# Optimization experiments

Measured on AMD Instinct MI355X. Metric: run time of the kernel, lower is better.

Reference implementation:

```python
import jax, jax.numpy as jnp
import numpy as np
import math

B, T, D, H = 2, 2048, 1024, 16
DH = D // H

def setup_inputs() -> dict:
    key = jax.random.key(0)
    ks = jax.random.split(key, 7)
    s = 0.02
    return {
        "q": jax.random.normal(ks[0], (B, T, D), jnp.float32),
        "k": jax.random.normal(ks[1], (B, T, D), jnp.float32),
        "v": jax.random.normal(ks[2], (B, T, D), jnp.float32),
        "wq": jax.random.normal(ks[3], (D, D), jnp.float32) * s,
        "wk": jax.random.normal(ks[4], (D, D), jnp.float32) * s,
        "wv": jax.random.normal(ks[5], (D, D), jnp.float32) * s,
        "wo": jax.random.normal(ks[6], (D, D), jnp.float32) * s,
    }

def reference(q, k, v, wq, wk, wv, wo):
    # nn.Linear(bias=False): y = x @ W.T
    qh = (q @ wq.T).reshape(B, T, H, DH).transpose(0, 2, 1, 3)  # [B,H,T,DH]
    kh = (k @ wk.T).reshape(B, T, H, DH).transpose(0, 2, 1, 3)
    vh = (v @ wv.T).reshape(B, T, H, DH).transpose(0, 2, 1, 3)
    scores = jnp.einsum('bhqd,bhkd->bhqk', qh, kh) / math.sqrt(DH)
    # causal mask: disallow j > i
    mask = jnp.triu(jnp.ones((T, T), dtype=bool), k=1)
    scores = jnp.where(mask[None, None], -jnp.inf, scores)
    attn = jax.nn.softmax(scores, axis=-1)  # dropout=0 (eval)
    out = jnp.einsum('bhqk,bhkd->bhqd', attn, vh)
    out = out.transpose(0, 2, 1, 3).reshape(B, T, D)
    return out @ wo.T
```

## Files before the change

### kernel.cpp

```cpp
#include <hip/hip_runtime.h>
#include <cstdint>
#include <cstddef>

#define B_  2
#define T_  2048
#define D_  1024
#define H_  16
#define DH_ 64
#define M_  (B_*T_)

typedef __bf16 bf16x8 __attribute__((ext_vector_type(8)));
typedef float  f32x4  __attribute__((ext_vector_type(4)));
typedef unsigned short us4 __attribute__((ext_vector_type(4)));
typedef unsigned short us8 __attribute__((ext_vector_type(8)));
typedef unsigned short ushort_t;

__device__ __forceinline__ unsigned short f32_to_bf16_rne(float f) {
    unsigned u = __builtin_bit_cast(unsigned, f);
    u += 0x7FFFu + ((u >> 16) & 1u);
    return (unsigned short)(u >> 16);
}

__device__ __forceinline__ unsigned pack_bf16_2(float f0, float f1) {
    unsigned a = __builtin_bit_cast(unsigned, f0) + 0x8000u;
    unsigned b = __builtin_bit_cast(unsigned, f1) + 0x8000u;
    return __builtin_amdgcn_perm(b, a, 0x07060302u);
}

__device__ __forceinline__ void async16(const void* g, void* l) {
    __builtin_amdgcn_global_load_lds(
        (const __attribute__((address_space(1))) unsigned int*)(uintptr_t)g,
        (__attribute__((address_space(3))) unsigned int*)(uintptr_t)l, 16, 0, 0);
}

__global__ __launch_bounds__(256) void cvt_all(
    const float* __restrict__ i0, const float* __restrict__ i1, const float* __restrict__ i2,
    const float* __restrict__ i3, const float* __restrict__ i4, const float* __restrict__ i5,
    const float* __restrict__ i6,
    ushort_t* __restrict__ o0, ushort_t* __restrict__ o1, ushort_t* __restrict__ o2,
    ushort_t* __restrict__ o3, ushort_t* __restrict__ o4, ushort_t* __restrict__ o5,
    ushort_t* __restrict__ o6) {
    const int y = blockIdx.y;
    const float* in = y == 0 ? i0 : y == 1 ? i1 : y == 2 ? i2 : y == 3 ? i3
                    : y == 4 ? i4 : y == 5 ? i5 : i6;
    ushort_t* out  = y == 0 ? o0 : y == 1 ? o1 : y == 2 ? o2 : y == 3 ? o3
                    : y == 4 ? o4 : y == 5 ? o5 : o6;
    const int n = (y < 3) ? (M_ * D_) : (D_ * D_);
    int i = (blockIdx.x * 256 + threadIdx.x) * 4;
    if (i >= n) return;
    float4 f = *reinterpret_cast<const float4*>(in + i);
    unsigned lo = pack_bf16_2(f.x, f.y);
    unsigned hi = pack_bf16_2(f.z, f.w);
    *reinterpret_cast<unsigned long long*>(out + i) =
        (unsigned long long)lo | ((unsigned long long)hi << 32);
}

__device__ __forceinline__ void gemm_mainloop(const ushort_t* __restrict__ A,
                                              const ushort_t* __restrict__ W,
                                              ushort_t* As, ushort_t* Bs,
                                              int m0, int n0, f32x4 acc[4][4]) {
    const int tid  = threadIdx.x;
    const int lc   = tid & 15;
    const int quad = (tid >> 4) & 3;
    const int wave = tid >> 6;
    const int wm = (wave >> 1) * 64, wn = (wave & 1) * 64;
    const int sw = lc & 7;

    const f32x4 fzero = {0.f, 0.f, 0.f, 0.f};
#pragma unroll
    for (int mt = 0; mt < 4; ++mt)
#pragma unroll
        for (int nt = 0; nt < 4; ++nt) acc[mt][nt] = fzero;

    for (int kk = 0; kk < D_; kk += 64) {
        __syncthreads();
#pragma unroll
        for (int i = 0; i < 4; ++i) {
            const int j = i * 256 + tid;
            const int r = j >> 3, c = (j & 7) ^ (r & 7);
            async16(A + (size_t)(m0 + r) * D_ + kk + c * 8, As + j * 8);
            async16(W + (size_t)(n0 + r) * D_ + kk + c * 8, Bs + j * 8);
        }
        __syncthreads();
#pragma unroll
        for (int ks = 0; ks < 2; ++ks) {
            bf16x8 af[4], bw[4];
#pragma unroll
            for (int mt = 0; mt < 4; ++mt)
                af[mt] = *reinterpret_cast<const bf16x8*>(
                    As + (wm + mt * 16 + lc) * 64 + (((ks * 4 + quad) ^ sw) * 8));
#pragma unroll
            for (int nt = 0; nt < 4; ++nt)
                bw[nt] = *reinterpret_cast<const bf16x8*>(
                    Bs + (wn + nt * 16 + lc) * 64 + (((ks * 4 + quad) ^ sw) * 8));
#pragma unroll
            for (int mt = 0; mt < 4; ++mt)
#pragma unroll
                for (int nt = 0; nt < 4; ++nt)
                    acc[mt][nt] = __builtin_amdgcn_mfma_f32_16x16x32_bf16(af[mt], bw[nt], acc[mt][nt], 0, 0, 0);
        }
    }
}

__global__ __launch_bounds__(256, 3) void gemm_qkv(
    const ushort_t* __restrict__ qb, const ushort_t* __restrict__ kb, const ushort_t* __restrict__ vb,
    const ushort_t* __restrict__ wqb, const ushort_t* __restrict__ wkb, const ushort_t* __restrict__ wvb,
    ushort_t* __restrict__ qhb, ushort_t* __restrict__ khb, ushort_t* __restrict__ vtb) {
    __shared__ __align__(16) ushort_t As[128 * 64];
    __shared__ __align__(16) ushort_t Bs[128 * 64];
    __shared__ __align__(16) ushort_t Ts[4][16 * 80];

    const int z = blockIdx.z;
    const ushort_t* A = z == 0 ? qb : z == 1 ? kb : vb;
    const ushort_t* W = z == 0 ? wqb : z == 1 ? wkb : wvb;
    const int yt = blockIdx.x + 8 * (blockIdx.y >> 3);
    const int xt = blockIdx.y & 7;
    const int m0 = yt * 128, n0 = xt * 128;

    f32x4 acc[4][4];
    gemm_mainloop(A, W, As, Bs, m0, n0, acc);

    const int tid = threadIdx.x, lane = tid & 63, lc = tid & 15;
    const int quad = (tid >> 4) & 3, wave = tid >> 6;
    const int wm = (wave >> 1) * 64, wn = (wave & 1) * 64;
    const int mG = m0 + wm;
    const int bb = mG >> 11, t0 = mG & (T_ - 1);
    const int hh = (n0 + wn) >> 6;

    if (z < 2) {
        ushort_t* outp = (z == 0 ? qhb : khb) + ((size_t)bb * H_ + hh) * T_ * DH_;
#pragma unroll
        for (int mt = 0; mt < 4; ++mt) {
#pragma unroll
            for (int nt = 0; nt < 4; ++nt)
#pragma unroll
                for (int r = 0; r < 4; ++r)
                    Ts[wave][(quad * 4 + r) * 80 + nt * 16 + lc] = f32_to_bf16_rne(acc[mt][nt][r]);
#pragma unroll
            for (int it = 0; it < 2; ++it) {
                const int c = it * 64 + lane;
                const int row = c >> 3, c8 = c & 7;
                us8 vv = *reinterpret_cast<const us8*>(Ts[wave] + row * 80 + c8 * 8);
                *reinterpret_cast<us8*>(outp + (size_t)(t0 + mt * 16 + row) * DH_ + c8 * 8) = vv;
            }
        }
    } else {
        ushort_t* base = vtb + ((size_t)bb * H_ + hh) * DH_ * T_;
#pragma unroll
        for (int mt = 0; mt < 4; ++mt) {
#pragma unroll
            for (int nt = 0; nt < 4; ++nt)
#pragma unroll
                for (int r = 0; r < 4; ++r)
                    Ts[wave][(nt * 16 + lc) * 16 + quad * 4 + r] = f32_to_bf16_rne(acc[mt][nt][r]);
#pragma unroll
            for (int it = 0; it < 2; ++it) {
                const int c = it * 64 + lane;
                const int nl = c >> 1, mh = c & 1;
                us8 vv = *reinterpret_cast<const us8*>(Ts[wave] + c * 8);
                *reinterpret_cast<us8*>(base + (size_t)nl * T_ + t0 + mt * 16 + mh * 8) = vv;
            }
        }
    }
}

__global__ __launch_bounds__(256, 4) void gemm_wo(const ushort_t* __restrict__ A,
                                                  const ushort_t* __restrict__ W,
                                                  float* __restrict__ out) {
    __shared__ __align__(16) ushort_t As[64 * 64];
    __shared__ __align__(16) ushort_t Bs[128 * 64];
    const int yt = blockIdx.x + 8 * (blockIdx.y >> 3);
    const int xt = blockIdx.y & 7;
    const int m0 = yt * 64, n0 = xt * 128;

    const int tid = threadIdx.x, lc = tid & 15;
    const int quad = (tid >> 4) & 3, wave = tid >> 6;
    const int wm = (wave >> 1) * 32, wn = (wave & 1) * 64;
    const int sw = lc & 7;

    const f32x4 fzero = {0.f, 0.f, 0.f, 0.f};
    f32x4 acc[2][4];
#pragma unroll
    for (int mt = 0; mt < 2; ++mt)
#pragma unroll
        for (int nt = 0; nt < 4; ++nt) acc[mt][nt] = fzero;

    for (int kk = 0; kk < D_; kk += 64) {
        __syncthreads();
#pragma unroll
        for (int i = 0; i < 2; ++i) {
            const int j = i * 256 + tid;
            const int r = j >> 3, c = (j & 7) ^ (r & 7);
            async16(A + (size_t)(m0 + r) * D_ + kk + c * 8, As + j * 8);
        }
#pragma unroll
        for (int i = 0; i < 4; ++i) {
            const int j = i * 256 + tid;
            const int r = j >> 3, c = (j & 7) ^ (r & 7);
            async16(W + (size_t)(n0 + r) * D_ + kk + c * 8, Bs + j * 8);
        }
        __syncthreads();
#pragma unroll
        for (int ks = 0; ks < 2; ++ks) {
            bf16x8 af[2], bw[4];
#pragma unroll
            for (int mt = 0; mt < 2; ++mt)
                af[mt] = *reinterpret_cast<const bf16x8*>(
                    As + (wm + mt * 16 + lc) * 64 + (((ks * 4 + quad) ^ sw) * 8));
#pragma unroll
            for (int nt = 0; nt < 4; ++nt)
                bw[nt] = *reinterpret_cast<const bf16x8*>(
                    Bs + (wn + nt * 16 + lc) * 64 + (((ks * 4 + quad) ^ sw) * 8));
#pragma unroll
            for (int mt = 0; mt < 2; ++mt)
#pragma unroll
                for (int nt = 0; nt < 4; ++nt)
                    acc[mt][nt] = __builtin_amdgcn_mfma_f32_16x16x32_bf16(af[mt], bw[nt], acc[mt][nt], 0, 0, 0);
        }
    }

#pragma unroll
    for (int mt = 0; mt < 2; ++mt)
#pragma unroll
        for (int nt = 0; nt < 4; ++nt)
#pragma unroll
            for (int r = 0; r < 4; ++r) {
                const int m = m0 + wm + mt * 16 + quad * 4 + r;
                const int n = n0 + wn + nt * 16 + lc;
                out[(size_t)m * D_ + n] = acc[mt][nt][r];
            }
}

__global__ __launch_bounds__(256, 3) void attn6(const ushort_t* __restrict__ Qh,
                                                const ushort_t* __restrict__ Kh,
                                                const ushort_t* __restrict__ Vt,
                                                ushort_t* __restrict__ Ao) {
    __shared__ __align__(16) ushort_t smem[16384 + 4 * 16 * 72];

    const int tid = threadIdx.x, lane = tid & 63, lc = tid & 15;
    const int quad = (tid >> 4) & 3, wave = tid >> 6;
    const int grp = wave >> 1, sub = wave & 1;
    const int sw = lc & 7;

    const int L = blockIdx.x;
    const int xcd = L & 7, s = L >> 3;
    const int qt = 31 - (s >> 2);
    const int bh = xcd + 8 * (s & 3);
    const int bb = bh >> 4, hh = bh & 15;
    const int q0 = qt * 64, nkt = qt + 1;
    const int nIt = (nkt + 1) >> 1;
    const int mbase = q0 + sub * 32;

    const ushort_t* Qp = Qh + (size_t)bh * T_ * DH_;
    const ushort_t* Kp = Kh + (size_t)bh * T_ * DH_;
    const ushort_t* Vp = Vt + (size_t)bh * DH_ * T_;
    const float SC2 = 0.18033688f;
    const f32x4 fzero = {0.f, 0.f, 0.f, 0.f};
    ushort_t* Pw = smem + 16384 + wave * (16 * 72);

    bf16x8 aq[2][2];
#pragma unroll
    for (int mt = 0; mt < 2; ++mt) {
        const ushort_t* qrow = Qp + (size_t)(mbase + mt * 16 + lc) * DH_ + quad * 8;
        aq[mt][0] = *reinterpret_cast<const bf16x8*>(qrow);
        aq[mt][1] = *reinterpret_cast<const bf16x8*>(qrow + 32);
    }

    f32x4 o[2][4];
    float lsum[2][4];
#pragma unroll
    for (int mt = 0; mt < 2; ++mt) {
#pragma unroll
        for (int ct = 0; ct < 4; ++ct) o[mt][ct] = fzero;
#pragma unroll
        for (int r = 0; r < 4; ++r) lsum[mt][r] = 0.f;
    }

    for (int it = 0; it < nIt; ++it) {
        const int kt0 = 2 * it;
        __syncthreads();
#pragma unroll
        for (int i = 0; i < 2; ++i) {
            const int j = i * 256 + tid;
            const int r = j >> 3, c = (j & 7) ^ (r & 7);
            const int kprm = 4 * (r & 15) + (r >> 4);
            async16(Kp + (size_t)(kt0 * 64 + kprm) * DH_ + c * 8, smem + j * 8);
            async16(Vp + (size_t)r * T_ + kt0 * 64 + c * 8,       smem + 8192 + j * 8);
            if (kt0 + 1 < nkt) {
                async16(Kp + (size_t)((kt0 + 1) * 64 + kprm) * DH_ + c * 8, smem + 4096 + j * 8);
                async16(Vp + (size_t)r * T_ + (kt0 + 1) * 64 + c * 8,       smem + 12288 + j * 8);
            }
        }
        __syncthreads();

        const int kt = kt0 + grp;
        if (kt < nkt) {
            const int k0 = kt * 64;
            const ushort_t* Kt    = smem + grp * 4096;
            const ushort_t* Vtile = smem + 8192 + grp * 4096;

            bf16x8 bv[4][2];
#pragma unroll
            for (int ct = 0; ct < 4; ++ct) {
                const ushort_t* vr = Vtile + (ct * 16 + lc) * 64;
                bv[ct][0] = *reinterpret_cast<const bf16x8*>(vr + ((quad ^ sw) * 8));
                bv[ct][1] = *reinterpret_cast<const bf16x8*>(vr + (((4 + quad) ^ sw) * 8));
            }

            f32x4 sc[2][4];
#pragma unroll
            for (int ct = 0; ct < 4; ++ct) {
                const ushort_t* kr = Kt + (ct * 16 + lc) * 64;
                bf16x8 bk0 = *reinterpret_cast<const bf16x8*>(kr + ((quad ^ sw) * 8));
                bf16x8 bk1 = *reinterpret_cast<const bf16x8*>(kr + (((4 + quad) ^ sw) * 8));
#pragma unroll
                for (int mt = 0; mt < 2; ++mt) {
                    sc[mt][ct] = __builtin_amdgcn_mfma_f32_16x16x32_bf16(aq[mt][0], bk0, fzero, 0, 0, 0);
                    sc[mt][ct] = __builtin_amdgcn_mfma_f32_16x16x32_bf16(aq[mt][1], bk1, sc[mt][ct], 0, 0, 0);
                }
            }

#pragma unroll
            for (int mt = 0; mt < 2; ++mt) {
                float e[4][4];
                if (kt == qt) {
#pragma unroll
                    for (int ct = 0; ct < 4; ++ct) {
                        const int key = k0 + 4 * lc + ct;
#pragma unroll
                        for (int r = 0; r < 4; ++r) {
                            const int row = mbase + mt * 16 + quad * 4 + r;
                            e[ct][r] = (key <= row) ? __builtin_amdgcn_exp2f(sc[mt][ct][r] * SC2) : 0.f;
                        }
                    }
                } else {
#pragma unroll
                    for (int ct = 0; ct < 4; ++ct)
#pragma unroll
                        for (int r = 0; r < 4; ++r)
                            e[ct][r] = __builtin_amdgcn_exp2f(sc[mt][ct][r] * SC2);
                }
#pragma unroll
                for (int r = 0; r < 4; ++r) {
                    lsum[mt][r] += (e[0][r] + e[1][r]) + (e[2][r] + e[3][r]);
                    unsigned lo = pack_bf16_2(e[0][r], e[1][r]);
                    unsigned hi = pack_bf16_2(e[2][r], e[3][r]);
                    *reinterpret_cast<unsigned long long*>(Pw + (quad * 4 + r) * 72 + lc * 4) =
                        (unsigned long long)lo | ((unsigned long long)hi << 32);
                }
                bf16x8 ap0 = *reinterpret_cast<const bf16x8*>(Pw + lc * 72 + quad * 8);
                bf16x8 ap1 = *reinterpret_cast<const bf16x8*>(Pw + lc * 72 + 32 + quad * 8);
#pragma unroll
                for (int ct = 0; ct < 4; ++ct) {
                    o[mt][ct] = __builtin_amdgcn_mfma_f32_16x16x32_bf16(ap0, bv[ct][0], o[mt][ct], 0, 0, 0);
                    o[mt][ct] = __builtin_amdgcn_mfma_f32_16x16x32_bf16(ap1, bv[ct][1], o[mt][ct], 0, 0, 0);
                }
            }
        }
    }

    __syncthreads();
    float* Osh = (float*)smem;
    float* Lsh = (float*)(smem + 8192);
    if (grp == 0) {
#pragma unroll
        for (int mt = 0; mt < 2; ++mt) {
#pragma unroll
            for (int ct = 0; ct < 4; ++ct)
#pragma unroll
                for (int r = 0; r < 4; ++r)
                    Osh[(sub * 32 + mt * 16 + quad * 4 + r) * 64 + ct * 16 + lc] = o[mt][ct][r];
#pragma unroll
            for (int r = 0; r < 4; ++r)
                Lsh[(sub * 32 + mt * 16 + quad * 4 + r) * 16 + lc] = lsum[mt][r];
        }
    }
    __syncthreads();
    if (grp == 1) {
#pragma unroll
        for (int mt = 0; mt < 2; ++mt) {
            float inv[4];
#pragma unroll
            for (int r = 0; r < 4; ++r) {
                float l = lsum[mt][r] + Lsh[(sub * 32 + mt * 16 + quad * 4 + r) * 16 + lc];
#pragma unroll
                for (int d = 1; d < 16; d <<= 1) l += __shfl_xor(l, d);
                inv[r] = 1.0f / l;
            }
#pragma unroll
            for (int ct = 0; ct < 4; ++ct)
#pragma unroll
                for (int r = 0; r < 4; ++r) {
                    const int rowq = mbase + mt * 16 + quad * 4 + r;
                    const float ov = o[mt][ct][r] +
                        Osh[(sub * 32 + mt * 16 + quad * 4 + r) * 64 + ct * 16 + lc];
                    Ao[((size_t)bb * T_ + rowq) * D_ + hh * DH_ + ct * 16 + lc] =
                        f32_to_bf16_rne(ov * inv[r]);
                }
        }
    }
}

extern "C" void kernel_launch(void* const* d_in, const int* in_sizes, int n_in,
                              void* d_out, int out_size, void* d_ws, size_t ws_size,
                              hipStream_t stream) {
    const float* q  = (const float*)d_in[0];
    const float* k  = (const float*)d_in[1];
    const float* v  = (const float*)d_in[2];
    const float* wq = (const float*)d_in[3];
    const float* wk = (const float*)d_in[4];
    const float* wv = (const float*)d_in[5];
    const float* wo = (const float*)d_in[6];

    char* ws = (char*)d_ws;
    size_t off = 0;
    auto alloc = [&](size_t bytes) -> char* {
        char* p = ws + off;
        off += (bytes + 255) & ~(size_t)255;
        return p;
    };
    ushort_t* qb  = (ushort_t*)alloc((size_t)M_ * D_ * 2);
    ushort_t* kb  = (ushort_t*)alloc((size_t)M_ * D_ * 2);
    ushort_t* vb  = (ushort_t*)alloc((size_t)M_ * D_ * 2);
    ushort_t* wqb = (ushort_t*)alloc((size_t)D_ * D_ * 2);
    ushort_t* wkb = (ushort_t*)alloc((size_t)D_ * D_ * 2);
    ushort_t* wvb = (ushort_t*)alloc((size_t)D_ * D_ * 2);
    ushort_t* wob = (ushort_t*)alloc((size_t)D_ * D_ * 2);
    ushort_t* qhb = (ushort_t*)alloc((size_t)M_ * D_ * 2);
    ushort_t* khb = (ushort_t*)alloc((size_t)M_ * D_ * 2);
    ushort_t* vtb = (ushort_t*)alloc((size_t)M_ * D_ * 2);
    ushort_t* aob = (ushort_t*)alloc((size_t)M_ * D_ * 2);

    cvt_all<<<dim3(4096, 7), 256, 0, stream>>>(q, k, v, wq, wk, wv, wo,
                                               qb, kb, vb, wqb, wkb, wvb, wob);

    gemm_qkv<<<dim3(8, 32, 3), 256, 0, stream>>>(qb, kb, vb, wqb, wkb, wvb, qhb, khb, vtb);

    attn6<<<dim3(1024), 256, 0, stream>>>(qhb, khb, vtb, aob);

    gemm_wo<<<dim3(8, 64), 256, 0, stream>>>(aob, wob, (float*)d_out);
}
```

Measured before the change: 187.5 us.

## Register-prefetch next K/V tiles, raise MFMA priority, coalesce attention output

The direct async global-to-LDS copies for each pair of K/V tiles are replaced by global loads into registers for the next iteration, issued before the current tile's compute and written to LDS between barriers, so memory latency overlaps with MFMA work. The MFMA sections are wrapped in s_setprio to favour matrix issue. The final bf16 output is staged through a swizzled LDS buffer so global stores become 16-byte coalesced rows instead of scattered 2-byte writes. In exchange it uses 32 more VGPRs for staging, which may press against the 3-blocks-per-CU launch bound, and adds an extra barrier and an LDS round trip at the end.

```diff
diff --git a/kernel.cpp b/kernel.cpp
--- a/kernel.cpp
+++ b/kernel.cpp
@@ -231,7 +231,7 @@
             }
 }
 
-__global__ __launch_bounds__(256, 3) void attn6(const ushort_t* __restrict__ Qh,
+__global__ __launch_bounds__(256, 3) void attn7(const ushort_t* __restrict__ Qh,
                                                 const ushort_t* __restrict__ Kh,
                                                 const ushort_t* __restrict__ Vt,
                                                 ushort_t* __restrict__ Ao) {
@@ -276,22 +276,48 @@
         for (int r = 0; r < 4; ++r) lsum[mt][r] = 0.f;
     }
 
+    us8 stg[8];
+    int jj[2], rr[2], cc[2], kprm[2];
+#pragma unroll
+    for (int i = 0; i < 2; ++i) {
+        jj[i] = i * 256 + tid;
+        rr[i] = jj[i] >> 3;
+        cc[i] = (jj[i] & 7) ^ (rr[i] & 7);
+        kprm[i] = 4 * (rr[i] & 15) + (rr[i] >> 4);
+    }
+
+#define LOAD_KV(IT)                                                                           \
+    {                                                                                         \
+        const int kt0n = 2 * (IT);                                                            \
+        const int kt1n = (kt0n + 1 < nkt) ? (kt0n + 1) : kt0n;                                \
+        _Pragma("unroll")                                                                     \
+        for (int i = 0; i < 2; ++i) {                                                         \
+            stg[i*4+0] = *reinterpret_cast<const us8*>(Kp + (size_t)(kt0n * 64 + kprm[i]) * DH_ + cc[i] * 8); \
+            stg[i*4+1] = *reinterpret_cast<const us8*>(Kp + (size_t)(kt1n * 64 + kprm[i]) * DH_ + cc[i] * 8); \
+            stg[i*4+2] = *reinterpret_cast<const us8*>(Vp + (size_t)rr[i] * T_ + kt0n * 64 + cc[i] * 8);      \
+            stg[i*4+3] = *reinterpret_cast<const us8*>(Vp + (size_t)rr[i] * T_ + kt1n * 64 + cc[i] * 8);      \
+        }                                                                                     \
+    }
+
+#define WRITE_KV()                                                                            \
+    {                                                                                         \
+        _Pragma("unroll")                                                                     \
+        for (int i = 0; i < 2; ++i) {                                                         \
+            *reinterpret_cast<us8*>(smem + jj[i] * 8)         = stg[i*4+0];                   \
+            *reinterpret_cast<us8*>(smem + 4096 + jj[i] * 8)  = stg[i*4+1];                   \
+            *reinterpret_cast<us8*>(smem + 8192 + jj[i] * 8)  = stg[i*4+2];                   \
+            *reinterpret_cast<us8*>(smem + 12288 + jj[i] * 8) = stg[i*4+3];                   \
+        }                                                                                     \
+    }
+
+    LOAD_KV(0);
+    WRITE_KV();
+    __syncthreads();
+
     for (int it = 0; it < nIt; ++it) {
         const int kt0 = 2 * it;
-        __syncthreads();
-#pragma unroll
-        for (int i = 0; i < 2; ++i) {
-            const int j = i * 256 + tid;
-            const int r = j >> 3, c = (j & 7) ^ (r & 7);
-            const int kprm = 4 * (r & 15) + (r >> 4);
-            async16(Kp + (size_t)(kt0 * 64 + kprm) * DH_ + c * 8, smem + j * 8);
-            async16(Vp + (size_t)r * T_ + kt0 * 64 + c * 8,       smem + 8192 + j * 8);
-            if (kt0 + 1 < nkt) {
-                async16(Kp + (size_t)((kt0 + 1) * 64 + kprm) * DH_ + c * 8, smem + 4096 + j * 8);
-                async16(Vp + (size_t)r * T_ + (kt0 + 1) * 64 + c * 8,       smem + 12288 + j * 8);
-            }
-        }
-        __syncthreads();
+        const bool hasNext = (it + 1 < nIt);
+        if (hasNext) LOAD_KV(it + 1);
 
         const int kt = kt0 + grp;
         if (kt < nkt) {
@@ -308,6 +334,7 @@
             }
 
             f32x4 sc[2][4];
+            __builtin_amdgcn_s_setprio(1);
 #pragma unroll
             for (int ct = 0; ct < 4; ++ct) {
                 const ushort_t* kr = Kt + (ct * 16 + lc) * 64;
@@ -319,6 +346,7 @@
                     sc[mt][ct] = __builtin_amdgcn_mfma_f32_16x16x32_bf16(aq[mt][1], bk1, sc[mt][ct], 0, 0, 0);
                 }
             }
+            __builtin_amdgcn_s_setprio(0);
 
 #pragma unroll
             for (int mt = 0; mt < 2; ++mt) {
@@ -350,18 +378,29 @@
                 }
                 bf16x8 ap0 = *reinterpret_cast<const bf16x8*>(Pw + lc * 72 + quad * 8);
                 bf16x8 ap1 = *reinterpret_cast<const bf16x8*>(Pw + lc * 72 + 32 + quad * 8);
+                __builtin_amdgcn_s_setprio(1);
 #pragma unroll
                 for (int ct = 0; ct < 4; ++ct) {
                     o[mt][ct] = __builtin_amdgcn_mfma_f32_16x16x32_bf16(ap0, bv[ct][0], o[mt][ct], 0, 0, 0);
                     o[mt][ct] = __builtin_amdgcn_mfma_f32_16x16x32_bf16(ap1, bv[ct][1], o[mt][ct], 0, 0, 0);
                 }
-            }
-        }
-    }
+                __builtin_amdgcn_s_setprio(0);
+            }
+        }
+
+        if (hasNext) {
+            __syncthreads();
+            WRITE_KV();
+            __syncthreads();
+        }
+    }
+#undef LOAD_KV
+#undef WRITE_KV
 
     __syncthreads();
     float* Osh = (float*)smem;
     float* Lsh = (float*)(smem + 8192);
+    ushort_t* Fsh = smem + 16384;
     if (grp == 0) {
 #pragma unroll
         for (int mt = 0; mt < 2; ++mt) {
@@ -391,13 +430,21 @@
             for (int ct = 0; ct < 4; ++ct)
 #pragma unroll
                 for (int r = 0; r < 4; ++r) {
-                    const int rowq = mbase + mt * 16 + quad * 4 + r;
-                    const float ov = o[mt][ct][r] +
-                        Osh[(sub * 32 + mt * 16 + quad * 4 + r) * 64 + ct * 16 + lc];
-                    Ao[((size_t)bb * T_ + rowq) * D_ + hh * DH_ + ct * 16 + lc] =
+                    const int row = sub * 32 + mt * 16 + quad * 4 + r;
+                    const float ov = o[mt][ct][r] + Osh[row * 64 + ct * 16 + lc];
+                    const int cu = ct * 16 + lc;
+                    Fsh[row * 64 + ((cu & 7) | ((((cu >> 3) ^ row) & 7) << 3))] =
                         f32_to_bf16_rne(ov * inv[r]);
                 }
         }
+    }
+    __syncthreads();
+#pragma unroll
+    for (int i = 0; i < 2; ++i) {
+        const int j = i * 256 + tid;
+        const int row = j >> 3, c8 = j & 7;
+        us8 vv = *reinterpret_cast<const us8*>(Fsh + row * 64 + ((c8 ^ row) & 7) * 8);
+        *reinterpret_cast<us8*>(Ao + ((size_t)bb * T_ + q0 + row) * D_ + hh * DH_ + c8 * 8) = vv;
     }
 }
 
@@ -436,7 +483,7 @@
 
     gemm_qkv<<<dim3(8, 32, 3), 256, 0, stream>>>(qb, kb, vb, wqb, wkb, wvb, qhb, khb, vtb);
 
-    attn6<<<dim3(1024), 256, 0, stream>>>(qhb, khb, vtb, aob);
+    attn7<<<dim3(1024), 256, 0, stream>>>(qhb, khb, vtb, aob);
 
     gemm_wo<<<dim3(8, 64), 256, 0, stream>>>(aob, wob, (float*)d_out);
 }
```

Result: slower. 246.4 us (+31.4%).

## Prefetch next K/V tiles into registers while computing, stage output through LDS

Applied to the files above, without the earlier changes.

The attention kernel replaces the async global-to-LDS copy followed by a barrier wait with register prefetching. The next pair of K/V tiles is loaded into registers while the current pair is computed, then written to LDS between barriers, so global load latency overlaps with MFMA work. MFMA sections are wrapped in s_setprio to favour matrix issue. The final bf16 output is staged through swizzled shared memory so it can be written with 16-byte coalesced stores instead of scattered 2-byte stores. The cost is more VGPRs for the prefetch buffers, which at launch bounds 256,3 risks spills or lower occupancy, plus an extra barrier per iteration.

```diff
diff --git a/kernel.cpp b/kernel.cpp
--- a/kernel.cpp
+++ b/kernel.cpp
@@ -231,13 +231,13 @@
             }
 }
 
-__global__ __launch_bounds__(256, 3) void attn6(const ushort_t* __restrict__ Qh,
+__global__ __launch_bounds__(256, 3) void attn8(const ushort_t* __restrict__ Qh,
                                                 const ushort_t* __restrict__ Kh,
                                                 const ushort_t* __restrict__ Vt,
                                                 ushort_t* __restrict__ Ao) {
     __shared__ __align__(16) ushort_t smem[16384 + 4 * 16 * 72];
 
-    const int tid = threadIdx.x, lane = tid & 63, lc = tid & 15;
+    const int tid = threadIdx.x, lc = tid & 15;
     const int quad = (tid >> 4) & 3, wave = tid >> 6;
     const int grp = wave >> 1, sub = wave & 1;
     const int sw = lc & 7;
@@ -276,92 +276,138 @@
         for (int r = 0; r < 4; ++r) lsum[mt][r] = 0.f;
     }
 
-    for (int it = 0; it < nIt; ++it) {
-        const int kt0 = 2 * it;
-        __syncthreads();
-#pragma unroll
-        for (int i = 0; i < 2; ++i) {
-            const int j = i * 256 + tid;
-            const int r = j >> 3, c = (j & 7) ^ (r & 7);
-            const int kprm = 4 * (r & 15) + (r >> 4);
-            async16(Kp + (size_t)(kt0 * 64 + kprm) * DH_ + c * 8, smem + j * 8);
-            async16(Vp + (size_t)r * T_ + kt0 * 64 + c * 8,       smem + 8192 + j * 8);
-            if (kt0 + 1 < nkt) {
-                async16(Kp + (size_t)((kt0 + 1) * 64 + kprm) * DH_ + c * 8, smem + 4096 + j * 8);
-                async16(Vp + (size_t)r * T_ + (kt0 + 1) * 64 + c * 8,       smem + 12288 + j * 8);
-            }
-        }
-        __syncthreads();
-
-        const int kt = kt0 + grp;
-        if (kt < nkt) {
-            const int k0 = kt * 64;
-            const ushort_t* Kt    = smem + grp * 4096;
-            const ushort_t* Vtile = smem + 8192 + grp * 4096;
-
-            bf16x8 bv[4][2];
+    const int jj0 = tid,        jj1 = 256 + tid;
+    const int rr0 = jj0 >> 3,   rr1 = jj1 >> 3;
+    const int cc0 = (jj0 & 7) ^ (rr0 & 7), cc1 = (jj1 & 7) ^ (rr1 & 7);
+    const int kp0 = 4 * (rr0 & 15) + (rr0 >> 4);
+    const int kp1 = 4 * (rr1 & 15) + (rr1 >> 4);
+    const ushort_t* pK0 = Kp + kp0 * DH_ + cc0 * 8;
+    const ushort_t* pK1 = Kp + kp1 * DH_ + cc1 * 8;
+    const ushort_t* pV0 = Vp + (size_t)rr0 * T_ + cc0 * 8;
+    const ushort_t* pV1 = Vp + (size_t)rr1 * T_ + cc1 * 8;
+
+    us8 sK0a, sK0b, sK1a, sK1b, sV0a, sV0b, sV1a, sV1b;
+
+#define LOAD_KV(T0, T1)                                                      \
+    {                                                                        \
+        sK0a = *reinterpret_cast<const us8*>(pK0 + (T0) * 4096);             \
+        sK0b = *reinterpret_cast<const us8*>(pK1 + (T0) * 4096);             \
+        sK1a = *reinterpret_cast<const us8*>(pK0 + (T1) * 4096);             \
+        sK1b = *reinterpret_cast<const us8*>(pK1 + (T1) * 4096);             \
+        sV0a = *reinterpret_cast<const us8*>(pV0 + (T0) * 64);               \
+        sV0b = *reinterpret_cast<const us8*>(pV1 + (T0) * 64);               \
+        sV1a = *reinterpret_cast<const us8*>(pV0 + (T1) * 64);               \
+        sV1b = *reinterpret_cast<const us8*>(pV1 + (T1) * 64);               \
+    }
+
+#define WRITE_KV()                                                           \
+    {                                                                        \
+        *reinterpret_cast<us8*>(smem + jj0 * 8)          = sK0a;             \
+        *reinterpret_cast<us8*>(smem + jj1 * 8)          = sK0b;             \
+        *reinterpret_cast<us8*>(smem + 4096 + jj0 * 8)   = sK1a;             \
+        *reinterpret_cast<us8*>(smem + 4096 + jj1 * 8)   = sK1b;             \
+        *reinterpret_cast<us8*>(smem + 8192 + jj0 * 8)   = sV0a;             \
+        *reinterpret_cast<us8*>(smem + 8192 + jj1 * 8)   = sV0b;             \
+        *reinterpret_cast<us8*>(smem + 12288 + jj0 * 8)  = sV1a;             \
+        *reinterpret_cast<us8*>(smem + 12288 + jj1 * 8)  = sV1b;             \
+    }
+
+    auto compute = [&](const int kt, const bool diag) {
+        const int k0 = kt * 64;
+        const ushort_t* Kt    = smem + grp * 4096;
+        const ushort_t* Vtile = smem + 8192 + grp * 4096;
+
+        bf16x8 bv[4][2];
+#pragma unroll
+        for (int ct = 0; ct < 4; ++ct) {
+            const ushort_t* vr = Vtile + (ct * 16 + lc) * 64;
+            bv[ct][0] = *reinterpret_cast<const bf16x8*>(vr + ((quad ^ sw) * 8));
+            bv[ct][1] = *reinterpret_cast<const bf16x8*>(vr + (((4 + quad) ^ sw) * 8));
+        }
+
+        f32x4 sc[2][4];
+        __builtin_amdgcn_s_setprio(1);
+#pragma unroll
+        for (int ct = 0; ct < 4; ++ct) {
+            const ushort_t* kr = Kt + (ct * 16 + lc) * 64;
+            bf16x8 bk0 = *reinterpret_cast<const bf16x8*>(kr + ((quad ^ sw) * 8));
+            bf16x8 bk1 = *reinterpret_cast<const bf16x8*>(kr + (((4 + quad) ^ sw) * 8));
+#pragma unroll
+            for (int mt = 0; mt < 2; ++mt) {
+                sc[mt][ct] = __builtin_amdgcn_mfma_f32_16x16x32_bf16(aq[mt][0], bk0, fzero, 0, 0, 0);
+                sc[mt][ct] = __builtin_amdgcn_mfma_f32_16x16x32_bf16(aq[mt][1], bk1, sc[mt][ct], 0, 0, 0);
+            }
+        }
+        __builtin_amdgcn_s_setprio(0);
+
+#pragma unroll
+        for (int mt = 0; mt < 2; ++mt) {
+            float e[4][4];
+            if (diag) {
+#pragma unroll
+                for (int ct = 0; ct < 4; ++ct) {
+                    const int key = k0 + 4 * lc + ct;
+#pragma unroll
+                    for (int r = 0; r < 4; ++r) {
+                        const int row = mbase + mt * 16 + quad * 4 + r;
+                        e[ct][r] = (key <= row) ? __builtin_amdgcn_exp2f(sc[mt][ct][r] * SC2) : 0.f;
+                    }
+                }
+            } else {
+#pragma unroll
+                for (int ct = 0; ct < 4; ++ct)
+#pragma unroll
+                    for (int r = 0; r < 4; ++r)
+                        e[ct][r] = __builtin_amdgcn_exp2f(sc[mt][ct][r] * SC2);
+            }
+#pragma unroll
+            for (int r = 0; r < 4; ++r) {
+                lsum[mt][r] += (e[0][r] + e[1][r]) + (e[2][r] + e[3][r]);
+                unsigned lo = pack_bf16_2(e[0][r], e[1][r]);
+                unsigned hi = pack_bf16_2(e[2][r], e[3][r]);
+                *reinterpret_cast<unsigned long long*>(Pw + (quad * 4 + r) * 72 + lc * 4) =
+                    (unsigned long long)lo | ((unsigned long long)hi << 32);
+            }
+            bf16x8 ap0 = *reinterpret_cast<const bf16x8*>(Pw + lc * 72 + quad * 8);
+            bf16x8 ap1 = *reinterpret_cast<const bf16x8*>(Pw + lc * 72 + 32 + quad * 8);
+            __builtin_amdgcn_s_setprio(1);
 #pragma unroll
             for (int ct = 0; ct < 4; ++ct) {
-                const ushort_t* vr = Vtile + (ct * 16 + lc) * 64;
-                bv[ct][0] = *reinterpret_cast<const bf16x8*>(vr + ((quad ^ sw) * 8));
-                bv[ct][1] = *reinterpret_cast<const bf16x8*>(vr + (((4 + quad) ^ sw) * 8));
-            }
-
-            f32x4 sc[2][4];
-#pragma unroll
-            for (int ct = 0; ct < 4; ++ct) {
-                const ushort_t* kr = Kt + (ct * 16 + lc) * 64;
-                bf16x8 bk0 = *reinterpret_cast<const bf16x8*>(kr + ((quad ^ sw) * 8));
-                bf16x8 bk1 = *reinterpret_cast<const bf16x8*>(kr + (((4 + quad) ^ sw) * 8));
-#pragma unroll
-                for (int mt = 0; mt < 2; ++mt) {
-                    sc[mt][ct] = __builtin_amdgcn_mfma_f32_16x16x32_bf16(aq[mt][0], bk0, fzero, 0, 0, 0);
-                    sc[mt][ct] = __builtin_amdgcn_mfma_f32_16x16x32_bf16(aq[mt][1], bk1, sc[mt][ct], 0, 0, 0);
-                }
-            }
-
-#pragma unroll
-            for (int mt = 0; mt < 2; ++mt) {
-                float e[4][4];
-                if (kt == qt) {
-#pragma unroll
-                    for (int ct = 0; ct < 4; ++ct) {
-                        const int key = k0 + 4 * lc + ct;
-#pragma unroll
-                        for (int r = 0; r < 4; ++r) {
-                            const int row = mbase + mt * 16 + quad * 4 + r;
-                            e[ct][r] = (key <= row) ? __builtin_amdgcn_exp2f(sc[mt][ct][r] * SC2) : 0.f;
-                        }
-                    }
-                } else {
-#pragma unroll
-                    for (int ct = 0; ct < 4; ++ct)
-#pragma unroll
-                        for (int r = 0; r < 4; ++r)
-                            e[ct][r] = __builtin_amdgcn_exp2f(sc[mt][ct][r] * SC2);
-                }
-#pragma unroll
-                for (int r = 0; r < 4; ++r) {
-                    lsum[mt][r] += (e[0][r] + e[1][r]) + (e[2][r] + e[3][r]);
-                    unsigned lo = pack_bf16_2(e[0][r], e[1][r]);
-                    unsigned hi = pack_bf16_2(e[2][r], e[3][r]);
-                    *reinterpret_cast<unsigned long long*>(Pw + (quad * 4 + r) * 72 + lc * 4) =
-                        (unsigned long long)lo | ((unsigned long long)hi << 32);
-                }
-                bf16x8 ap0 = *reinterpret_cast<const bf16x8*>(Pw + lc * 72 + quad * 8);
-                bf16x8 ap1 = *reinterpret_cast<const bf16x8*>(Pw + lc * 72 + 32 + quad * 8);
-#pragma unroll
-                for (int ct = 0; ct < 4; ++ct) {
-                    o[mt][ct] = __builtin_amdgcn_mfma_f32_16x16x32_bf16(ap0, bv[ct][0], o[mt][ct], 0, 0, 0);
-                    o[mt][ct] = __builtin_amdgcn_mfma_f32_16x16x32_bf16(ap1, bv[ct][1], o[mt][ct], 0, 0, 0);
-                }
-            }
-        }
-    }
+                o[mt][ct] = __builtin_amdgcn_mfma_f32_16x16x32_bf16(ap0, bv[ct][0], o[mt][ct], 0, 0, 0);
+                o[mt][ct] = __builtin_amdgcn_mfma_f32_16x16x32_bf16(ap1, bv[ct][1], o[mt][ct], 0, 0, 0);
+            }
+            __builtin_amdgcn_s_setprio(0);
+        }
+    };
+
+    {
+        const int t1 = (nkt > 1) ? 1 : 0;
+        LOAD_KV(0, t1);
+        WRITE_KV();
+        __syncthreads();
+    }
+
+    for (int it = 0; it < nIt - 1; ++it) {
+        const int n0t = 2 * it + 2;
+        const int n1t = (n0t + 1 < nkt) ? n0t + 1 : n0t;
+        LOAD_KV(n0t, n1t);
+        compute(2 * it + grp, false);
+        __syncthreads();
+        WRITE_KV();
+        __syncthreads();
+    }
+
+    {
+        const int ktL = 2 * (nIt - 1) + grp;
+        if (ktL < nkt) compute(ktL, ktL == qt);
+    }
+#undef LOAD_KV
+#undef WRITE_KV
 
     __syncthreads();
     float* Osh = (float*)smem;
     float* Lsh = (float*)(smem + 8192);
+    ushort_t* Fsh = smem + 16384;
     if (grp == 0) {
 #pragma unroll
         for (int mt = 0; mt < 2; ++mt) {
@@ -391,13 +437,21 @@
             for (int ct = 0; ct < 4; ++ct)
 #pragma unroll
                 for (int r = 0; r < 4; ++r) {
-                    const int rowq = mbase + mt * 16 + quad * 4 + r;
-                    const float ov = o[mt][ct][r] +
-                        Osh[(sub * 32 + mt * 16 + quad * 4 + r) * 64 + ct * 16 + lc];
-                    Ao[((size_t)bb * T_ + rowq) * D_ + hh * DH_ + ct * 16 + lc] =
+                    const int row = sub * 32 + mt * 16 + quad * 4 + r;
+                    const float ov = o[mt][ct][r] + Osh[row * 64 + ct * 16 + lc];
+                    const int cu = ct * 16 + lc;
+                    Fsh[row * 64 + ((cu & 7) | ((((cu >> 3) ^ row) & 7) << 3))] =
                         f32_to_bf16_rne(ov * inv[r]);
                 }
         }
+    }
+    __syncthreads();
+#pragma unroll
+    for (int i = 0; i < 2; ++i) {
+        const int j = i * 256 + tid;
+        const int row = j >> 3, c8 = j & 7;
+        us8 vv = *reinterpret_cast<const us8*>(Fsh + row * 64 + ((c8 ^ row) & 7) * 8);
+        *reinterpret_cast<us8*>(Ao + ((size_t)bb * T_ + q0 + row) * D_ + hh * DH_ + c8 * 8) = vv;
     }
 }
 
@@ -436,7 +490,7 @@
 
     gemm_qkv<<<dim3(8, 32, 3), 256, 0, stream>>>(qb, kb, vb, wqb, wkb, wvb, qhb, khb, vtb);
 
-    attn6<<<dim3(1024), 256, 0, stream>>>(qhb, khb, vtb, aob);
+    attn8<<<dim3(1024), 256, 0, stream>>>(qhb, khb, vtb, aob);
 
     gemm_wo<<<dim3(8, 64), 256, 0, stream>>>(aob, wob, (float*)d_out);
 }
```

After: 198.6 us. 5.9% more time.

## Load K/V fragments directly from global in attention, drop shared staging

Applied to the files above, without the earlier changes.

The attention kernel no longer stages K and V tiles in shared memory behind block-wide barriers. Each wave group now reads its K and V MFMA operands straight from global memory (relying on L2/L1) and walks alternating key tiles with no synchronisation inside the loop. It also adds s_setprio around the MFMA bursts, swizzles the P scratch layout, and stages the output through LDS for 16-byte coalesced stores. Launch bounds drop to 2 blocks per CU. The trade is barrier and LDS-copy overhead removed against uncoalesced global loads with higher latency exposure.

```diff
diff --git a/kernel.cpp b/kernel.cpp
--- a/kernel.cpp
+++ b/kernel.cpp
@@ -231,16 +231,15 @@
             }
 }
 
-__global__ __launch_bounds__(256, 3) void attn6(const ushort_t* __restrict__ Qh,
-                                                const ushort_t* __restrict__ Kh,
-                                                const ushort_t* __restrict__ Vt,
-                                                ushort_t* __restrict__ Ao) {
-    __shared__ __align__(16) ushort_t smem[16384 + 4 * 16 * 72];
-
-    const int tid = threadIdx.x, lane = tid & 63, lc = tid & 15;
+__global__ __launch_bounds__(256, 2) void attn12(const ushort_t* __restrict__ Qh,
+                                                 const ushort_t* __restrict__ Kh,
+                                                 const ushort_t* __restrict__ Vt,
+                                                 ushort_t* __restrict__ Ao) {
+    __shared__ __align__(16) ushort_t smem[14336];
+
+    const int tid = threadIdx.x, lc = tid & 15;
     const int quad = (tid >> 4) & 3, wave = tid >> 6;
     const int grp = wave >> 1, sub = wave & 1;
-    const int sw = lc & 7;
 
     const int L = blockIdx.x;
     const int xcd = L & 7, s = L >> 3;
@@ -248,7 +247,6 @@
     const int bh = xcd + 8 * (s & 3);
     const int bb = bh >> 4, hh = bh & 15;
     const int q0 = qt * 64, nkt = qt + 1;
-    const int nIt = (nkt + 1) >> 1;
     const int mbase = q0 + sub * 32;
 
     const ushort_t* Qp = Qh + (size_t)bh * T_ * DH_;
@@ -256,7 +254,7 @@
     const ushort_t* Vp = Vt + (size_t)bh * DH_ * T_;
     const float SC2 = 0.18033688f;
     const f32x4 fzero = {0.f, 0.f, 0.f, 0.f};
-    ushort_t* Pw = smem + 16384 + wave * (16 * 72);
+    ushort_t* Pw = smem + 10240 + wave * 1024;
 
     bf16x8 aq[2][2];
 #pragma unroll
@@ -276,92 +274,96 @@
         for (int r = 0; r < 4; ++r) lsum[mt][r] = 0.f;
     }
 
-    for (int it = 0; it < nIt; ++it) {
-        const int kt0 = 2 * it;
-        __syncthreads();
-#pragma unroll
-        for (int i = 0; i < 2; ++i) {
-            const int j = i * 256 + tid;
-            const int r = j >> 3, c = (j & 7) ^ (r & 7);
-            const int kprm = 4 * (r & 15) + (r >> 4);
-            async16(Kp + (size_t)(kt0 * 64 + kprm) * DH_ + c * 8, smem + j * 8);
-            async16(Vp + (size_t)r * T_ + kt0 * 64 + c * 8,       smem + 8192 + j * 8);
-            if (kt0 + 1 < nkt) {
-                async16(Kp + (size_t)((kt0 + 1) * 64 + kprm) * DH_ + c * 8, smem + 4096 + j * 8);
-                async16(Vp + (size_t)r * T_ + (kt0 + 1) * 64 + c * 8,       smem + 12288 + j * 8);
-            }
-        }
-        __syncthreads();
-
-        const int kt = kt0 + grp;
-        if (kt < nkt) {
-            const int k0 = kt * 64;
-            const ushort_t* Kt    = smem + grp * 4096;
-            const ushort_t* Vtile = smem + 8192 + grp * 4096;
-
-            bf16x8 bv[4][2];
+    const ushort_t* pK[4];
+    const ushort_t* pV[4];
+#pragma unroll
+    for (int ct = 0; ct < 4; ++ct) {
+        pK[ct] = Kp + (size_t)(4 * lc + ct) * DH_ + quad * 8;
+        pV[ct] = Vp + (size_t)(ct * 16 + lc) * T_ + quad * 8;
+    }
+
+    auto compute = [&](const int kt, const bool diag) {
+        const int k0 = kt * 64;
+
+        bf16x8 bk[4][2];
+#pragma unroll
+        for (int ct = 0; ct < 4; ++ct) {
+            const ushort_t* kr = pK[ct] + (size_t)kt * 4096;
+            bk[ct][0] = *reinterpret_cast<const bf16x8*>(kr);
+            bk[ct][1] = *reinterpret_cast<const bf16x8*>(kr + 32);
+        }
+
+        f32x4 sc[2][4];
+        __builtin_amdgcn_s_setprio(1);
+#pragma unroll
+        for (int ct = 0; ct < 4; ++ct)
+#pragma unroll
+            for (int mt = 0; mt < 2; ++mt) {
+                sc[mt][ct] = __builtin_amdgcn_mfma_f32_16x16x32_bf16(aq[mt][0], bk[ct][0], fzero, 0, 0, 0);
+                sc[mt][ct] = __builtin_amdgcn_mfma_f32_16x16x32_bf16(aq[mt][1], bk[ct][1], sc[mt][ct], 0, 0, 0);
+            }
+        __builtin_amdgcn_s_setprio(0);
+
+        bf16x8 bv[4][2];
+#pragma unroll
+        for (int ct = 0; ct < 4; ++ct) {
+            const ushort_t* vr = pV[ct] + k0;
+            bv[ct][0] = *reinterpret_cast<const bf16x8*>(vr);
+            bv[ct][1] = *reinterpret_cast<const bf16x8*>(vr + 32);
+        }
+
+#pragma unroll
+        for (int mt = 0; mt < 2; ++mt) {
+            float e[4][4];
+            if (diag) {
+#pragma unroll
+                for (int ct = 0; ct < 4; ++ct) {
+                    const int key = k0 + 4 * lc + ct;
+#pragma unroll
+                    for (int r = 0; r < 4; ++r) {
+                        const int row = mbase + mt * 16 + quad * 4 + r;
+                        e[ct][r] = (key <= row) ? __builtin_amdgcn_exp2f(sc[mt][ct][r] * SC2) : 0.f;
+                    }
+                }
+            } else {
+#pragma unroll
+                for (int ct = 0; ct < 4; ++ct)
+#pragma unroll
+                    for (int r = 0; r < 4; ++r)
+                        e[ct][r] = __builtin_amdgcn_exp2f(sc[mt][ct][r] * SC2);
+            }
+#pragma unroll
+            for (int r = 0; r < 4; ++r) {
+                lsum[mt][r] += (e[0][r] + e[1][r]) + (e[2][r] + e[3][r]);
+                unsigned lo = pack_bf16_2(e[0][r], e[1][r]);
+                unsigned hi = pack_bf16_2(e[2][r], e[3][r]);
+                const int row = quad * 4 + r;
+                const int punit = (lc >> 1) ^ (row & 7);
+                *reinterpret_cast<unsigned long long*>(
+                    Pw + row * 64 + punit * 8 + (lc & 1) * 4) =
+                    (unsigned long long)lo | ((unsigned long long)hi << 32);
+            }
+            bf16x8 ap0 = *reinterpret_cast<const bf16x8*>(
+                Pw + lc * 64 + ((quad ^ (lc & 7)) * 8));
+            bf16x8 ap1 = *reinterpret_cast<const bf16x8*>(
+                Pw + lc * 64 + (((4 + quad) ^ (lc & 7)) * 8));
+            __builtin_amdgcn_s_setprio(1);
 #pragma unroll
             for (int ct = 0; ct < 4; ++ct) {
-                const ushort_t* vr = Vtile + (ct * 16 + lc) * 64;
-                bv[ct][0] = *reinterpret_cast<const bf16x8*>(vr + ((quad ^ sw) * 8));
-                bv[ct][1] = *reinterpret_cast<const bf16x8*>(vr + (((4 + quad) ^ sw) * 8));
-            }
-
-            f32x4 sc[2][4];
-#pragma unroll
-            for (int ct = 0; ct < 4; ++ct) {
-                const ushort_t* kr = Kt + (ct * 16 + lc) * 64;
-                bf16x8 bk0 = *reinterpret_cast<const bf16x8*>(kr + ((quad ^ sw) * 8));
-                bf16x8 bk1 = *reinterpret_cast<const bf16x8*>(kr + (((4 + quad) ^ sw) * 8));
-#pragma unroll
-                for (int mt = 0; mt < 2; ++mt) {
-                    sc[mt][ct] = __builtin_amdgcn_mfma_f32_16x16x32_bf16(aq[mt][0], bk0, fzero, 0, 0, 0);
-                    sc[mt][ct] = __builtin_amdgcn_mfma_f32_16x16x32_bf16(aq[mt][1], bk1, sc[mt][ct], 0, 0, 0);
-                }
-            }
-
-#pragma unroll
-            for (int mt = 0; mt < 2; ++mt) {
-                float e[4][4];
-                if (kt == qt) {
-#pragma unroll
-                    for (int ct = 0; ct < 4; ++ct) {
-                        const int key = k0 + 4 * lc + ct;
-#pragma unroll
-                        for (int r = 0; r < 4; ++r) {
-                            const int row = mbase + mt * 16 + quad * 4 + r;
-                            e[ct][r] = (key <= row) ? __builtin_amdgcn_exp2f(sc[mt][ct][r] * SC2) : 0.f;
-                        }
-                    }
-                } else {
-#pragma unroll
-                    for (int ct = 0; ct < 4; ++ct)
-#pragma unroll
-                        for (int r = 0; r < 4; ++r)
-                            e[ct][r] = __builtin_amdgcn_exp2f(sc[mt][ct][r] * SC2);
-                }
-#pragma unroll
-                for (int r = 0; r < 4; ++r) {
-                    lsum[mt][r] += (e[0][r] + e[1][r]) + (e[2][r] + e[3][r]);
-                    unsigned lo = pack_bf16_2(e[0][r], e[1][r]);
-                    unsigned hi = pack_bf16_2(e[2][r], e[3][r]);
-                    *reinterpret_cast<unsigned long long*>(Pw + (quad * 4 + r) * 72 + lc * 4) =
-                        (unsigned long long)lo | ((unsigned long long)hi << 32);
-                }
-                bf16x8 ap0 = *reinterpret_cast<const bf16x8*>(Pw + lc * 72 + quad * 8);
-                bf16x8 ap1 = *reinterpret_cast<const bf16x8*>(Pw + lc * 72 + 32 + quad * 8);
-#pragma unroll
-                for (int ct = 0; ct < 4; ++ct) {
-                    o[mt][ct] = __builtin_amdgcn_mfma_f32_16x16x32_bf16(ap0, bv[ct][0], o[mt][ct], 0, 0, 0);
-                    o[mt][ct] = __builtin_amdgcn_mfma_f32_16x16x32_bf16(ap1, bv[ct][1], o[mt][ct], 0, 0, 0);
-                }
-            }
-        }
-    }
+                o[mt][ct] = __builtin_amdgcn_mfma_f32_16x16x32_bf16(ap0, bv[ct][0], o[mt][ct], 0, 0, 0);
+                o[mt][ct] = __builtin_amdgcn_mfma_f32_16x16x32_bf16(ap1, bv[ct][1], o[mt][ct], 0, 0, 0);
+            }
+            __builtin_amdgcn_s_setprio(0);
+        }
+    };
+
+    for (int kt = grp; kt < qt; kt += 2) compute(kt, false);
+    if ((qt & 1) == grp) compute(qt, true);
 
     __syncthreads();
     float* Osh = (float*)smem;
     float* Lsh = (float*)(smem + 8192);
+    ushort_t* Fsh = smem + 10240;
     if (grp == 0) {
 #pragma unroll
         for (int mt = 0; mt < 2; ++mt) {
@@ -391,13 +393,21 @@
             for (int ct = 0; ct < 4; ++ct)
 #pragma unroll
                 for (int r = 0; r < 4; ++r) {
-                    const int rowq = mbase + mt * 16 + quad * 4 + r;
-                    const float ov = o[mt][ct][r] +
-                        Osh[(sub * 32 + mt * 16 + quad * 4 + r) * 64 + ct * 16 + lc];
-                    Ao[((size_t)bb * T_ + rowq) * D_ + hh * DH_ + ct * 16 + lc] =
+                    const int row = sub * 32 + mt * 16 + quad * 4 + r;
+                    const float ov = o[mt][ct][r] + Osh[row * 64 + ct * 16 + lc];
+                    const int cu = ct * 16 + lc;
+                    Fsh[row * 64 + ((cu & 7) | ((((cu >> 3) ^ row) & 7) << 3))] =
                         f32_to_bf16_rne(ov * inv[r]);
                 }
         }
+    }
+    __syncthreads();
+#pragma unroll
+    for (int i = 0; i < 2; ++i) {
+        const int j = i * 256 + tid;
+        const int row = j >> 3, c8 = j & 7;
+        us8 vv = *reinterpret_cast<const us8*>(Fsh + row * 64 + ((c8 ^ row) & 7) * 8);
+        *reinterpret_cast<us8*>(Ao + ((size_t)bb * T_ + q0 + row) * D_ + hh * DH_ + c8 * 8) = vv;
     }
 }
 
@@ -436,7 +446,7 @@
 
     gemm_qkv<<<dim3(8, 32, 3), 256, 0, stream>>>(qb, kb, vb, wqb, wkb, wvb, qhb, khb, vtb);
 
-    attn6<<<dim3(1024), 256, 0, stream>>>(qhb, khb, vtb, aob);
+    attn12<<<dim3(1024), 256, 0, stream>>>(qhb, khb, vtb, aob);
 
     gemm_wo<<<dim3(8, 64), 256, 0, stream>>>(aob, wob, (float*)d_out);
 }
```

Result: slower. 227.4 us (+21.3%).
